# Kernel optimization log

Hardware: AMD Instinct MI355X
Metric: run time of the kernel (lower is better)

The kernel has to match this reference:

```python
import jax, jax.numpy as jnp
import numpy as np

N = 50000      # num nodes
E = 800000     # num edges (before self loops)
HID = 64       # hidden_channels
HEADS = 4
B = 256        # num graphs in batch
TEXT, VIS, AUD = 768, 512, 128


def setup_inputs() -> dict:
    key = jax.random.key(0)
    ks = jax.random.split(key, 24)
    rn = lambda k, shape: jax.random.normal(k, shape, dtype=jnp.float32) * 0.05
    inp = {}
    inp["x"] = jax.random.normal(ks[0], (N, TEXT), dtype=jnp.float32)
    inp["node_type"] = jax.random.randint(ks[1], (N,), 0, 3, dtype=jnp.int32)
    inp["edge_index"] = jax.random.randint(ks[2], (2, E), 0, N, dtype=jnp.int32)
    inp["batch"] = jnp.sort(jax.random.randint(ks[3], (N,), 0, B, dtype=jnp.int32))
    # modality projections
    inp["Wt"] = rn(ks[4], (TEXT, HID)); inp["bt"] = jnp.zeros((HID,), jnp.float32)
    inp["Wv"] = rn(ks[5], (VIS, HID));  inp["bv"] = jnp.zeros((HID,), jnp.float32)
    inp["Wa"] = rn(ks[6], (AUD, HID));  inp["ba"] = jnp.zeros((HID,), jnp.float32)
    # GATConv1: in=HID, out=HID, heads=HEADS, concat=True
    inp["W1"]  = rn(ks[7], (HID, HEADS * HID))
    inp["a1s"] = rn(ks[8], (HEADS, HID))
    inp["a1d"] = rn(ks[9], (HEADS, HID))
    inp["b1"]  = jnp.zeros((HEADS * HID,), jnp.float32)
    # GATConv2: in=HID*HEADS, out=HID, heads=1, concat=False
    inp["W2"]  = rn(ks[10], (HID * HEADS, HID))
    inp["a2s"] = rn(ks[11], (1, HID))
    inp["a2d"] = rn(ks[12], (1, HID))
    inp["b2"]  = jnp.zeros((HID,), jnp.float32)
    # final classifier (num_classes==2 -> out_dim 1, squeezed)
    inp["Wl"] = rn(ks[13], (HID, 1)); inp["bl"] = jnp.zeros((1,), jnp.float32)
    return inp


def gat_conv(x, edge_index, W, a_src, a_dst, bias, concat):
    """PyG-style GATConv (eval mode, add_self_loops=True, shared lin for src/dst)."""
    n = x.shape[0]
    heads, c = a_src.shape
    loops = jnp.arange(n, dtype=edge_index.dtype)
    src = jnp.concatenate([edge_index[0], loops])
    dst = jnp.concatenate([edge_index[1], loops])
    h = (x @ W).reshape(n, heads, c)                       # [N, H, C]
    alpha_s = jnp.einsum('nhc,hc->nh', h, a_src)           # [N, H]
    alpha_d = jnp.einsum('nhc,hc->nh', h, a_dst)
    e = jax.nn.leaky_relu(alpha_s[src] + alpha_d[dst], 0.2)  # [E', H]
    # numerically-stable softmax over incoming edges of each dst node
    m = jax.ops.segment_max(e, dst, num_segments=n)
    e = jnp.exp(e - m[dst])
    denom = jax.ops.segment_sum(e, dst, num_segments=n)
    alpha = e / (denom[dst] + 1e-16)                        # [E', H]
    out = jax.ops.segment_sum(h[src] * alpha[:, :, None], dst, num_segments=n)
    out = out.reshape(n, heads * c) if concat else out.mean(axis=1)
    return out + bias


def reference(x, node_type, edge_index, batch,
              Wt, bt, Wv, bv, Wa, ba,
              W1, a1s, a1d, b1, W2, a2s, a2d, b2, Wl, bl):
    # masked multimodal projection (type 0=text, 1=vision, 2=audio)
    t = x[:, :TEXT] @ Wt + bt
    v = x[:, :VIS] @ Wv + bv
    a = x[:, :AUD] @ Wa + ba
    nt = node_type[:, None]
    h = jnp.where(nt == 0, t, jnp.where(nt == 1, v, a))     # [N, HID]
    h = jax.nn.elu(gat_conv(h, edge_index, W1, a1s, a1d, b1, concat=True))
    h = gat_conv(h, edge_index, W2, a2s, a2d, b2, concat=False)  # [N, HID]
    # global mean pool over graphs
    sums = jax.ops.segment_sum(h, batch, num_segments=B)
    cnts = jax.ops.segment_sum(jnp.ones((h.shape[0], 1), h.dtype), batch, num_segments=B)
    g = sums / jnp.maximum(cnts, 1.0)                       # [B, HID]
    out = (g @ Wl + bl).squeeze(-1)                          # [B] (binary logit)
    return out
```

## Files before the change

kernel.cpp:

```cpp
#include <hip/hip_runtime.h>
#include <cstdint>
#include <cstddef>

#define TEXTD 768
#define VISD  512
#define AUDD  128

__device__ __forceinline__ float wred_sum(float v){
  #pragma unroll
  for (int m = 32; m >= 1; m >>= 1) v += __shfl_xor(v, m, 64);
  return v;
}
__device__ __forceinline__ float wred_max(float v){
  #pragma unroll
  for (int m = 32; m >= 1; m >>= 1) v = fmaxf(v, __shfl_xor(v, m, 64));
  return v;
}

__global__ __launch_bounds__(256) void k_bcount(const int* __restrict__ ntype, int nN, int nblk,
                                                int* __restrict__ bcnt, int* __restrict__ deg){
  int b = blockIdx.x;
  int i = b*256 + threadIdx.x;
  int lane = threadIdx.x & 63, w = threadIdx.x >> 6;
  int ty = (i < nN) ? ntype[i] : -1;
  if (i < nN) deg[i] = 1;
  __shared__ int wc[4][3];
  #pragma unroll
  for (int t = 0; t < 3; t++){
    unsigned long long m = __ballot(ty == t);
    if (lane == 0) wc[w][t] = __popcll(m);
  }
  __syncthreads();
  if (threadIdx.x < 3){
    int t = threadIdx.x;
    bcnt[t*nblk + b] = wc[0][t] + wc[1][t] + wc[2][t] + wc[3][t];
  }
}
__global__ __launch_bounds__(1024) void k_bscan(const int* __restrict__ bcnt, int nblk, int nN,
                                                int* __restrict__ boff, int* __restrict__ toff,
                                                int* __restrict__ tcnt){
  __shared__ int s[2048];
  int n3 = nblk*3;
  int t = threadIdx.x;
  for (int i = t; i < n3; i += 1024) s[i] = bcnt[i];
  __syncthreads();
  if (t == 0){
    int run = 0;
    for (int i = 0; i < n3; i++){ int v = s[i]; s[i] = run; run += v; }
  }
  __syncthreads();
  for (int i = t; i < n3; i += 1024) boff[i] = s[i];
  if (t == 0){
    toff[0] = 0;         toff[1] = s[nblk];           toff[2] = s[2*nblk];
    tcnt[0] = s[nblk];   tcnt[1] = s[2*nblk]-s[nblk]; tcnt[2] = nN - s[2*nblk];
  }
}
__global__ __launch_bounds__(256) void k_bscatter(const int* __restrict__ ntype, int nN, int nblk,
                                                  const int* __restrict__ boff, int* __restrict__ order){
  int b = blockIdx.x;
  int i = b*256 + threadIdx.x;
  int lane = threadIdx.x & 63, w = threadIdx.x >> 6;
  int ty = (i < nN) ? ntype[i] : -1;
  __shared__ int wc[4][3];
  __shared__ int woff[4][3];
  unsigned long long masks[3];
  #pragma unroll
  for (int t = 0; t < 3; t++){
    masks[t] = __ballot(ty == t);
    if (lane == 0) wc[w][t] = __popcll(masks[t]);
  }
  __syncthreads();
  if (threadIdx.x < 3){
    int t = threadIdx.x, run = 0;
    #pragma unroll
    for (int ww = 0; ww < 4; ww++){ woff[ww][t] = run; run += wc[ww][t]; }
  }
  __syncthreads();
  if (ty >= 0){
    int r = __popcll(masks[ty] & ((1ULL << lane) - 1ULL));
    int pos = boff[ty*nblk + b] + woff[w][ty] + r;
    order[pos] = i;
  }
}

__global__ void k_deg_edges(const int* __restrict__ ei, int E, int* __restrict__ deg){
  int i = blockIdx.x*blockDim.x + threadIdx.x;
  if (i < E) atomicAdd(&deg[ei[E + i]], 1);
}
__global__ __launch_bounds__(1024) void k_scan(int* __restrict__ deg, int* __restrict__ off, int n){
  __shared__ int wsum[16];
  __shared__ int carry_s;
  int t = threadIdx.x, lane = t & 63, w = t >> 6;
  if (t == 0) carry_s = 0;
  __syncthreads();
  for (int base = 0; base < n; base += 1024){
    int i = base + t;
    int v = (i < n) ? deg[i] : 0;
    int orig = v;
    #pragma unroll
    for (int o = 1; o < 64; o <<= 1){ int u = __shfl_up(v, o, 64); if (lane >= o) v += u; }
    if (lane == 63) wsum[w] = v;
    __syncthreads();
    if (t < 16){
      int xv = wsum[t];
      #pragma unroll
      for (int o = 1; o < 16; o <<= 1){ int u = __shfl_up(xv, o, 16); if (t >= o) xv += u; }
      wsum[t] = xv;
    }
    __syncthreads();
    int wbase = (w == 0) ? 0 : wsum[w-1];
    int incl = v + wbase;
    int carry = carry_s;
    if (i < n){ int e = carry + incl - orig; off[i] = e; deg[i] = e; }
    __syncthreads();
    if (t == 0) carry_s = carry + wsum[15];
    __syncthreads();
  }
  if (threadIdx.x == 0) off[n] = carry_s;
}
__global__ void k_scatter(const int* __restrict__ ei, int E, int nN,
                          int* __restrict__ pos, int* __restrict__ csr_src){
  int i = blockIdx.x*blockDim.x + threadIdx.x;
  int total = E + nN;
  if (i >= total) return;
  int s, d;
  if (i < E){ s = ei[i]; d = ei[E + i]; } else { s = i - E; d = s; }
  int p = atomicAdd(&pos[d], 1);
  csr_src[p] = s;
}

__global__ __launch_bounds__(256) void k_afold(const float* __restrict__ W1,
    const float* __restrict__ a1s, const float* __restrict__ a1d,
    float* __restrict__ wfs, float* __restrict__ wfd){
  int t = threadIdx.x;
  int k = t & 63, h = t >> 6;
  const float* wr = W1 + (size_t)k*256 + h*64;
  const float* as = a1s + h*64;
  const float* ad = a1d + h*64;
  float s = 0.f, d = 0.f;
  for (int c = 0; c < 64; c += 4){
    float4 w  = *reinterpret_cast<const float4*>(wr + c);
    float4 sa = *reinterpret_cast<const float4*>(as + c);
    float4 da = *reinterpret_cast<const float4*>(ad + c);
    s += w.x*sa.x + w.y*sa.y + w.z*sa.z + w.w*sa.w;
    d += w.x*da.x + w.y*da.y + w.z*da.z + w.w*da.w;
  }
  wfs[k*4 + h] = s;
  wfd[k*4 + h] = d;
}

__global__ __launch_bounds__(256) void k_projgemm(const float* __restrict__ x,
    const int* __restrict__ order, const int* __restrict__ toff, const int* __restrict__ tcnt,
    const float* __restrict__ Wt, const float* __restrict__ bt,
    const float* __restrict__ Wv, const float* __restrict__ bv,
    const float* __restrict__ Wa, const float* __restrict__ ba,
    const float* __restrict__ wfs, const float* __restrict__ wfd,
    float* __restrict__ h0, float* __restrict__ as1, float* __restrict__ ad1){
  int ty = blockIdx.y;
  int cnt = tcnt[ty];
  int tile = blockIdx.x;
  if (tile*64 >= cnt) return;
  const float* W; const float* bias; int dim;
  if (ty == 0)      { W = Wt; bias = bt; dim = TEXTD; }
  else if (ty == 1) { W = Wv; bias = bv; dim = VISD; }
  else              { W = Wa; bias = ba; dim = AUDD; }
  int off = toff[ty];

  __shared__ float xsT[64][68];
  __shared__ float ws [64][68];
  __shared__ int   nid[64];

  int t = threadIdx.x;
  if (t < 64){
    int idx = tile*64 + t;
    nid[t] = (idx < cnt) ? order[off + idx] : -1;
  }
  __syncthreads();

  int node_l = t & 63;
  int ndl = nid[node_l];
  const float* xrow = x + (size_t)(ndl < 0 ? 0 : ndl) * TEXTD;
  int wrow = t >> 2, wu = t & 3;
  int wvq  = t >> 6;
  int n0 = (t & 15)*4, c0 = (t >> 4)*4, qg = t >> 4;
  float acc[4][4] = {};

  for (int k0 = 0; k0 < dim; k0 += 64){
    __syncthreads();
    #pragma unroll
    for (int j = 0; j < 4; j++){
      int f4 = wvq*4 + j;
      float4 v = *reinterpret_cast<const float4*>(xrow + k0 + f4*4);
      xsT[f4*4+0][node_l] = v.x;
      xsT[f4*4+1][node_l] = v.y;
      xsT[f4*4+2][node_l] = v.z;
      xsT[f4*4+3][node_l] = v.w;
    }
    #pragma unroll
    for (int j = 0; j < 4; j++){
      int f4 = j*4 + wu;
      float4 v = *reinterpret_cast<const float4*>(W + (size_t)(k0 + wrow)*64 + f4*4);
      *reinterpret_cast<float4*>(&ws[wrow][f4*4]) = v;
    }
    __syncthreads();
    #pragma unroll 8
    for (int kk = 0; kk < 64; kk++){
      float4 xv = *reinterpret_cast<const float4*>(&xsT[kk][n0]);
      float4 wv = *reinterpret_cast<const float4*>(&ws[kk][c0]);
      float xa[4] = {xv.x, xv.y, xv.z, xv.w};
      float wb[4] = {wv.x, wv.y, wv.z, wv.w};
      #pragma unroll
      for (int i = 0; i < 4; i++)
        #pragma unroll
        for (int j = 0; j < 4; j++)
          acc[i][j] += xa[i] * wb[j];
    }
  }

  float4 b4 = *reinterpret_cast<const float4*>(bias + c0);
  float bb[4] = {b4.x, b4.y, b4.z, b4.w};
  #pragma unroll
  for (int i = 0; i < 4; i++){
    int nd = nid[n0 + i];
    if (nd >= 0){
      float4 o4 = make_float4(acc[i][0]+bb[0], acc[i][1]+bb[1], acc[i][2]+bb[2], acc[i][3]+bb[3]);
      *reinterpret_cast<float4*>(h0 + (size_t)nd*64 + c0) = o4;
    }
  }

  __syncthreads();
  float* spart = &ws [0][0];
  float* dpart = &xsT[0][0];
  float4 wsv[4], wdv[4];
  #pragma unroll
  for (int j = 0; j < 4; j++){
    wsv[j] = *reinterpret_cast<const float4*>(wfs + (c0+j)*4);
    wdv[j] = *reinterpret_cast<const float4*>(wfd + (c0+j)*4);
  }
  #pragma unroll
  for (int i = 0; i < 4; i++){
    float hv[4];
    #pragma unroll
    for (int j = 0; j < 4; j++) hv[j] = acc[i][j] + bb[j];
    float s0v = hv[0]*wsv[0].x + hv[1]*wsv[1].x + hv[2]*wsv[2].x + hv[3]*wsv[3].x;
    float s1v = hv[0]*wsv[0].y + hv[1]*wsv[1].y + hv[2]*wsv[2].y + hv[3]*wsv[3].y;
    float s2v = hv[0]*wsv[0].z + hv[1]*wsv[1].z + hv[2]*wsv[2].z + hv[3]*wsv[3].z;
    float s3v = hv[0]*wsv[0].w + hv[1]*wsv[1].w + hv[2]*wsv[2].w + hv[3]*wsv[3].w;
    float d0v = hv[0]*wdv[0].x + hv[1]*wdv[1].x + hv[2]*wdv[2].x + hv[3]*wdv[3].x;
    float d1v = hv[0]*wdv[0].y + hv[1]*wdv[1].y + hv[2]*wdv[2].y + hv[3]*wdv[3].y;
    float d2v = hv[0]*wdv[0].z + hv[1]*wdv[1].z + hv[2]*wdv[2].z + hv[3]*wdv[3].z;
    float d3v = hv[0]*wdv[0].w + hv[1]*wdv[1].w + hv[2]*wdv[2].w + hv[3]*wdv[3].w;
    int nidx = (n0 + i)*64 + qg*4;
    spart[nidx+0]=s0v; spart[nidx+1]=s1v; spart[nidx+2]=s2v; spart[nidx+3]=s3v;
    dpart[nidx+0]=d0v; dpart[nidx+1]=d1v; dpart[nidx+2]=d2v; dpart[nidx+3]=d3v;
  }
  __syncthreads();
  if (t < 64){
    int nd = nid[t];
    if (nd >= 0){
      float s[4] = {0,0,0,0}, d[4] = {0,0,0,0};
      #pragma unroll
      for (int g = 0; g < 16; g++){
        #pragma unroll
        for (int h = 0; h < 4; h++){
          s[h] += spart[t*64 + g*4 + h];
          d[h] += dpart[t*64 + g*4 + h];
        }
      }
      *reinterpret_cast<float4*>(as1 + (size_t)nd*4) = make_float4(s[0],s[1],s[2],s[3]);
      *reinterpret_cast<float4*>(ad1 + (size_t)nd*4) = make_float4(d[0],d[1],d[2],d[3]);
    }
  }
}

__global__ __launch_bounds__(256) void k_gat1z(const int* __restrict__ off, const int* __restrict__ srcs,
    const float* __restrict__ as1, const float* __restrict__ ad1,
    const float* __restrict__ h0, float* __restrict__ z, int nN){
  int w = threadIdx.x >> 6, L = threadIdx.x & 63;
  int n = blockIdx.x*4 + w;
  __shared__ int   s_src[4][64];
  __shared__ float s_p[4][64][4];
  if (n >= nN) return;
  int hL = L >> 4, c4 = (L & 15)*4;
  float ad[4];
  { float4 a = *reinterpret_cast<const float4*>(ad1 + (size_t)n*4);
    ad[0]=a.x; ad[1]=a.y; ad[2]=a.z; ad[3]=a.w; }
  int s0 = off[n], s1 = off[n+1];
  float m[4] = {-1e30f,-1e30f,-1e30f,-1e30f};
  float den[4] = {0.f,0.f,0.f,0.f};
  float4 acc = make_float4(0.f,0.f,0.f,0.f);
  for (int base = s0; base < s1; base += 64){
    int e = base + L;
    int cl = min(64, s1 - base);
    bool valid = (e < s1);
    int sv = 0; float v[4];
    if (valid){
      sv = srcs[e];
      float4 a = *reinterpret_cast<const float4*>(as1 + (size_t)sv*4);
      float av[4] = {a.x,a.y,a.z,a.w};
      #pragma unroll
      for (int h = 0; h < 4; h++){ float tt = av[h] + ad[h]; v[h] = (tt>0.f)?tt:0.2f*tt; }
    } else {
      #pragma unroll
      for (int h = 0; h < 4; h++) v[h] = -1e30f;
    }
    float sc[4], pv[4];
    #pragma unroll
    for (int h = 0; h < 4; h++){
      float cm = wred_max(v[h]);
      float mn = fmaxf(m[h], cm);
      sc[h] = __expf(m[h] - mn);
      m[h] = mn;
      float p = valid ? __expf(v[h] - mn) : 0.f;
      den[h] = den[h]*sc[h] + wred_sum(p);
      pv[h] = p;
    }
    { float s4 = sc[hL]; acc.x*=s4; acc.y*=s4; acc.z*=s4; acc.w*=s4; }
    if (valid){
      s_src[w][L] = sv;
      *reinterpret_cast<float4*>(&s_p[w][L][0]) = make_float4(pv[0],pv[1],pv[2],pv[3]);
    }
    #pragma unroll 4
    for (int e2 = 0; e2 < cl; e2++){
      int sr = s_src[w][e2];
      float pp = s_p[w][e2][hL];
      float4 hv = *reinterpret_cast<const float4*>(h0 + (size_t)sr*64 + c4);
      acc.x += pp*hv.x; acc.y += pp*hv.y; acc.z += pp*hv.z; acc.w += pp*hv.w;
    }
  }
  float dl = den[hL] + 1e-16f;
  *reinterpret_cast<float4*>(z + (size_t)n*256 + hL*64 + c4) =
      make_float4(acc.x/dl, acc.y/dl, acc.z/dl, acc.w/dl);
}

__global__ __launch_bounds__(256) void k_glin1(const float* __restrict__ z,
    const float* __restrict__ W1, const float* __restrict__ b1,
    float* __restrict__ g1, int nN){
  int tile = blockIdx.x, q = blockIdx.y;
  int base = tile*64;
  __shared__ float xsT[64][68];
  __shared__ float ws [64][68];
  int t = threadIdx.x;
  int row = t >> 2, fq = t & 3;
  {
    int nd = base + row; if (nd >= nN) nd = nN - 1;
    const float* zr = z + (size_t)nd*256 + q*64;
    #pragma unroll
    for (int j = 0; j < 4; j++){
      int f4 = j*4 + fq;
      float4 v = *reinterpret_cast<const float4*>(zr + f4*4);
      xsT[f4*4+0][row] = v.x; xsT[f4*4+1][row] = v.y;
      xsT[f4*4+2][row] = v.z; xsT[f4*4+3][row] = v.w;
    }
  }
  #pragma unroll
  for (int j = 0; j < 4; j++){
    int f4 = j*4 + fq;
    float4 v = *reinterpret_cast<const float4*>(W1 + (size_t)row*256 + q*64 + f4*4);
    *reinterpret_cast<float4*>(&ws[row][f4*4]) = v;
  }
  __syncthreads();

  int n0 = (t & 15)*4, c0 = (t >> 4)*4;
  float acc[4][4] = {};
  #pragma unroll 8
  for (int k = 0; k < 64; k++){
    float4 xv = *reinterpret_cast<const float4*>(&xsT[k][n0]);
    float4 wv = *reinterpret_cast<const float4*>(&ws[k][c0]);
    float xa[4] = {xv.x, xv.y, xv.z, xv.w};
    float wb[4] = {wv.x, wv.y, wv.z, wv.w};
    #pragma unroll
    for (int i = 0; i < 4; i++)
      #pragma unroll
      for (int j = 0; j < 4; j++)
        acc[i][j] += xa[i] * wb[j];
  }
  float4 b4 = *reinterpret_cast<const float4*>(b1 + q*64 + c0);
  float bb[4] = {b4.x, b4.y, b4.z, b4.w};
  #pragma unroll
  for (int i = 0; i < 4; i++){
    int nd = base + n0 + i;
    if (nd < nN){
      float o[4];
      #pragma unroll
      for (int j = 0; j < 4; j++){
        float u = acc[i][j] + bb[j];
        o[j] = (u > 0.f) ? u : expm1f(u);
      }
      *reinterpret_cast<float4*>(g1 + (size_t)nd*256 + q*64 + c0) =
          make_float4(o[0], o[1], o[2], o[3]);
    }
  }
}

__global__ __launch_bounds__(256) void k_lin2t(const float* __restrict__ g1,
    const float* __restrict__ W2, const float* __restrict__ a2s, const float* __restrict__ a2d,
    float* __restrict__ h2, float* __restrict__ as2, float* __restrict__ ad2, int nN){
  int tile = blockIdx.x;
  int base = tile*64;
  __shared__ float xsT[64][68];
  __shared__ float ws [64][68];
  __shared__ float sPart[16][64];
  __shared__ float dPart[16][64];

  int t = threadIdx.x;
  int row = t >> 2, fq = t & 3;
  int ndl = base + row; if (ndl >= nN) ndl = nN - 1;
  const float* gr = g1 + (size_t)ndl*256;
  int n0 = (t & 15)*4, c0 = (t >> 4)*4, qg = t >> 4;
  float acc[4][4] = {};

  for (int k0 = 0; k0 < 256; k0 += 64){
    __syncthreads();
    #pragma unroll
    for (int j = 0; j < 4; j++){
      int f4 = j*4 + fq;
      float4 v = *reinterpret_cast<const float4*>(gr + k0 + f4*4);
      xsT[f4*4+0][row] = v.x; xsT[f4*4+1][row] = v.y;
      xsT[f4*4+2][row] = v.z; xsT[f4*4+3][row] = v.w;
    }
    #pragma unroll
    for (int j = 0; j < 4; j++){
      int f4 = j*4 + fq;
      float4 v = *reinterpret_cast<const float4*>(W2 + (size_t)(k0 + row)*64 + f4*4);
      *reinterpret_cast<float4*>(&ws[row][f4*4]) = v;
    }
    __syncthreads();
    #pragma unroll 8
    for (int k = 0; k < 64; k++){
      float4 xv = *reinterpret_cast<const float4*>(&xsT[k][n0]);
      float4 wv = *reinterpret_cast<const float4*>(&ws[k][c0]);
      float xa[4] = {xv.x, xv.y, xv.z, xv.w};
      float wb[4] = {wv.x, wv.y, wv.z, wv.w};
      #pragma unroll
      for (int i = 0; i < 4; i++)
        #pragma unroll
        for (int j = 0; j < 4; j++)
          acc[i][j] += xa[i] * wb[j];
    }
  }

  float avs[4], avd[4];
  {
    float4 s4 = *reinterpret_cast<const float4*>(a2s + c0);
    float4 d4 = *reinterpret_cast<const float4*>(a2d + c0);
    avs[0]=s4.x; avs[1]=s4.y; avs[2]=s4.z; avs[3]=s4.w;
    avd[0]=d4.x; avd[1]=d4.y; avd[2]=d4.z; avd[3]=d4.w;
  }
  #pragma unroll
  for (int i = 0; i < 4; i++){
    int nd = base + n0 + i;
    float sp = acc[i][0]*avs[0] + acc[i][1]*avs[1] + acc[i][2]*avs[2] + acc[i][3]*avs[3];
    float dp = acc[i][0]*avd[0] + acc[i][1]*avd[1] + acc[i][2]*avd[2] + acc[i][3]*avd[3];
    sPart[qg][n0+i] = sp;
    dPart[qg][n0+i] = dp;
    if (nd < nN){
      float4 o4 = make_float4(acc[i][0], acc[i][1], acc[i][2], acc[i][3]);
      *reinterpret_cast<float4*>(h2 + (size_t)nd*64 + c0) = o4;
    }
  }
  __syncthreads();
  if (t < 64){
    int nd = base + t;
    if (nd < nN){
      float s = 0.f, d = 0.f;
      #pragma unroll
      for (int g = 0; g < 16; g++){ s += sPart[g][t]; d += dPart[g][t]; }
      as2[nd] = s;
      ad2[nd] = d;
    }
  }
}

__global__ __launch_bounds__(256) void k_gat2v(const int* __restrict__ off, const int* __restrict__ srcs,
    const float* __restrict__ as2, const float* __restrict__ ad2,
    const float* __restrict__ h2, const float* __restrict__ b2,
    float* __restrict__ g2, int nN){
  int w = threadIdx.x >> 6, L = threadIdx.x & 63;
  int n = blockIdx.x*4 + w;
  if (n >= nN) return;
  int g = L >> 4, c4 = (L & 15)*4;
  float ad = ad2[n];
  int s0 = off[n], s1 = off[n+1];
  float m = -1e30f, den = 0.f;
  float4 acc = make_float4(0.f,0.f,0.f,0.f);
  for (int base = s0; base < s1; base += 64){
    int e = base + L;
    int cl = min(64, s1 - base);
    bool valid = (e < s1);
    int sv = 0; float v = -1e30f;
    if (valid){
      sv = srcs[e];
      float tt = as2[sv] + ad;
      v = (tt>0.f)?tt:0.2f*tt;
    }
    float cm = wred_max(v);
    float mn = fmaxf(m, cm);
    float sc = __expf(m - mn);
    m = mn;
    float p = valid ? __expf(v - mn) : 0.f;
    den = den*sc + wred_sum(p);
    acc.x*=sc; acc.y*=sc; acc.z*=sc; acc.w*=sc;
    int iters = (cl + 3) >> 2;
    for (int it = 0; it < iters; ++it){
      int e2   = it*4 + g;
      int esrc = (e2 < cl) ? e2 : (cl - 1);
      int   sr = __shfl(sv, esrc, 64);
      float pp = __shfl(p,  esrc, 64);
      if (e2 < cl){
        float4 hv = *reinterpret_cast<const float4*>(h2 + (size_t)sr*64 + c4);
        acc.x += pp*hv.x; acc.y += pp*hv.y; acc.z += pp*hv.z; acc.w += pp*hv.w;
      }
    }
  }
  #pragma unroll
  for (int s = 16; s <= 32; s <<= 1){
    acc.x += __shfl_xor(acc.x, s, 64);
    acc.y += __shfl_xor(acc.y, s, 64);
    acc.z += __shfl_xor(acc.z, s, 64);
    acc.w += __shfl_xor(acc.w, s, 64);
  }
  float dl = den + 1e-16f;
  if (L < 16){
    float4 b4 = *reinterpret_cast<const float4*>(b2 + c4);
    float4 o4 = make_float4(acc.x/dl + b4.x, acc.y/dl + b4.y,
                            acc.z/dl + b4.z, acc.w/dl + b4.w);
    *reinterpret_cast<float4*>(g2 + (size_t)n*64 + c4) = o4;
  }
}

__global__ void k_bstart(const int* __restrict__ batch, int nN, int B, int* __restrict__ bstart){
  int i = blockIdx.x*blockDim.x + threadIdx.x;
  if (i < nN){
    int prev = (i == 0) ? -1 : batch[i-1];
    int cur  = batch[i];
    for (int b = prev+1; b <= cur; b++) bstart[b] = i;
  } else if (i == nN){
    int last = batch[nN-1];
    for (int b = last+1; b <= B; b++) bstart[b] = nN;
  }
}

__global__ __launch_bounds__(64) void k_pool(const float* __restrict__ g2, const int* __restrict__ bstart,
    const float* __restrict__ Wl, const float* __restrict__ bl, float* __restrict__ out, int B){
  int b = blockIdx.x, c = threadIdx.x;
  int r0 = bstart[b], r1 = bstart[b+1];
  float s = 0.f;
  int i = r0;
  for (; i + 4 <= r1; i += 4){
    s += g2[(size_t)(i+0)*64 + c];
    s += g2[(size_t)(i+1)*64 + c];
    s += g2[(size_t)(i+2)*64 + c];
    s += g2[(size_t)(i+3)*64 + c];
  }
  for (; i < r1; i++) s += g2[(size_t)i*64 + c];
  float g = s / fmaxf((float)(r1 - r0), 1.f);
  float v = wred_sum(g * Wl[c]);
  if (c == 0) out[b] = v + bl[0];
}

extern "C" void kernel_launch(void* const* d_in, const int* in_sizes, int n_in,
                              void* d_out, int out_size, void* d_ws, size_t ws_size,
                              hipStream_t stream){
  const float* x    = (const float*)d_in[0];
  const int*   ntyp = (const int*)  d_in[1];
  const int*   ei   = (const int*)  d_in[2];
  const int*   batch= (const int*)  d_in[3];
  const float* Wt = (const float*)d_in[4];
  const float* bt = (const float*)d_in[5];
  const float* Wv = (const float*)d_in[6];
  const float* bv = (const float*)d_in[7];
  const float* Wa = (const float*)d_in[8];
  const float* ba = (const float*)d_in[9];
  const float* W1 = (const float*)d_in[10];
  const float* a1s= (const float*)d_in[11];
  const float* a1d= (const float*)d_in[12];
  const float* b1 = (const float*)d_in[13];
  const float* W2 = (const float*)d_in[14];
  const float* a2s= (const float*)d_in[15];
  const float* a2d= (const float*)d_in[16];
  const float* b2 = (const float*)d_in[17];
  const float* Wl = (const float*)d_in[18];
  const float* bl = (const float*)d_in[19];

  const int N = in_sizes[1];
  const int E = in_sizes[2] / 2;
  const int B = out_size;
  const int nblk = (N + 255)/256;

  char* ws = (char*)d_ws;
  size_t o = 0;
  auto alloc = [&](size_t bytes) -> void* {
    void* p = ws + o;
    o = (o + bytes + 255) & ~(size_t)255;
    return p;
  };
  int*   csr_off = (int*)  alloc((size_t)(N+1)*4);
  int*   pos     = (int*)  alloc((size_t)N*4);
  int*   csr_src = (int*)  alloc((size_t)(E+N)*4);
  float* as1     = (float*)alloc((size_t)N*4*4);
  float* ad1     = (float*)alloc((size_t)N*4*4);
  float* h0      = (float*)alloc((size_t)N*64*4);
  float* zbuf    = (float*)alloc((size_t)N*256*4);
  float* g1      = (float*)alloc((size_t)N*256*4);
  int*   bstart  = (int*)  alloc((size_t)(B+1)*4);
  int*   bcnt    = (int*)  alloc((size_t)nblk*3*4);
  int*   boff    = (int*)  alloc((size_t)nblk*3*4);
  int*   toff    = (int*)  alloc(3*4);
  int*   tcnt    = (int*)  alloc(3*4);
  int*   order   = (int*)  alloc((size_t)N*4);
  float* wfs     = (float*)alloc(256*4);
  float* wfd     = (float*)alloc(256*4);
  float* h2  = h0;
  float* as2 = as1;
  float* ad2 = ad1;
  float* g2  = zbuf;

  k_bcount  <<<nblk, 256, 0, stream>>>(ntyp, N, nblk, bcnt, pos);
  k_bscan   <<<1, 1024, 0, stream>>>(bcnt, nblk, N, boff, toff, tcnt);
  k_bscatter<<<nblk, 256, 0, stream>>>(ntyp, N, nblk, boff, order);

  k_deg_edges<<<(E + 255)/256, 256, 0, stream>>>(ei, E, pos);
  k_scan     <<<1, 1024, 0, stream>>>(pos, csr_off, N);
  k_scatter  <<<(E + N + 255)/256, 256, 0, stream>>>(ei, E, N, pos, csr_src);

  k_bstart<<<(N + 1 + 255)/256, 256, 0, stream>>>(batch, N, B, bstart);

  k_afold<<<1, 256, 0, stream>>>(W1, a1s, a1d, wfs, wfd);

  {
    dim3 g((N + 63)/64, 3);
    k_projgemm<<<g, 256, 0, stream>>>(x, order, toff, tcnt, Wt, bt, Wv, bv, Wa, ba,
                                      wfs, wfd, h0, as1, ad1);
  }

  k_gat1z <<<(N + 3)/4, 256, 0, stream>>>(csr_off, csr_src, as1, ad1, h0, zbuf, N);
  {
    dim3 g((N + 63)/64, 4);
    k_glin1<<<g, 256, 0, stream>>>(zbuf, W1, b1, g1, N);
  }

  k_lin2t<<<(N + 63)/64, 256, 0, stream>>>(g1, W2, a2s, a2d, h2, as2, ad2, N);
  k_gat2v<<<(N + 3)/4, 256, 0, stream>>>(csr_off, csr_src, as2, ad2, h2, b2, g2, N);
  k_pool<<<B, 64, 0, stream>>>(g2, bstart, Wl, bl, (float*)d_out, B);
}
```

Baseline: 390.7 us.

## Fuse GAT1 linear+ELU into layer-2 GEMM and parallelize degree scan

The GAT1 output projection (z·W1 + b1, ELU) is now computed per 64-column chunk in shared memory and fed straight into the W2 GEMM inside one kernel. This removes the 50000x256 g1 intermediate, which was written and then read back in full. The single-block serial prefix scan over node degrees becomes a three-kernel block-sum, small-scan and offset-write scheme that uses many blocks. The trade-offs are extra syncs and smem traffic per chunk in the fused kernel, fewer launched blocks for the first GEMM, and two extra small launches.

```diff
diff --git a/kernel.cpp b/kernel.cpp
--- a/kernel.cpp
+++ b/kernel.cpp
@@ -7,6 +7,11 @@
 #define AUDD  128
 
 __device__ __forceinline__ float wred_sum(float v){
+  #pragma unroll
+  for (int m = 32; m >= 1; m >>= 1) v += __shfl_xor(v, m, 64);
+  return v;
+}
+__device__ __forceinline__ int wred_sumi(int v){
   #pragma unroll
   for (int m = 32; m >= 1; m >>= 1) v += __shfl_xor(v, m, 64);
   return v;
@@ -87,36 +92,53 @@
   int i = blockIdx.x*blockDim.x + threadIdx.x;
   if (i < E) atomicAdd(&deg[ei[E + i]], 1);
 }
-__global__ __launch_bounds__(1024) void k_scan(int* __restrict__ deg, int* __restrict__ off, int n){
+__global__ __launch_bounds__(1024) void k_sumblk(const int* __restrict__ deg, int n,
+                                                 int* __restrict__ bsum){
+  int b = blockIdx.x;
+  int i = b*1024 + threadIdx.x;
+  int lane = threadIdx.x & 63, w = threadIdx.x >> 6;
   __shared__ int wsum[16];
-  __shared__ int carry_s;
+  int v = (i < n) ? deg[i] : 0;
+  v = wred_sumi(v);
+  if (lane == 0) wsum[w] = v;
+  __syncthreads();
+  if (threadIdx.x == 0){
+    int s = 0;
+    #pragma unroll
+    for (int k = 0; k < 16; k++) s += wsum[k];
+    bsum[b] = s;
+  }
+}
+__global__ void k_sumscan(const int* __restrict__ bsum, int nsb, int* __restrict__ bsoff){
+  if (threadIdx.x == 0){
+    int run = 0;
+    for (int i = 0; i < nsb; i++){ bsoff[i] = run; run += bsum[i]; }
+    bsoff[nsb] = run;
+  }
+}
+__global__ __launch_bounds__(1024) void k_offw(int* __restrict__ deg, const int* __restrict__ bsoff,
+                                               int n, int* __restrict__ off){
+  int b = blockIdx.x;
+  int i = b*1024 + threadIdx.x;
   int t = threadIdx.x, lane = t & 63, w = t >> 6;
-  if (t == 0) carry_s = 0;
-  __syncthreads();
-  for (int base = 0; base < n; base += 1024){
-    int i = base + t;
-    int v = (i < n) ? deg[i] : 0;
-    int orig = v;
-    #pragma unroll
-    for (int o = 1; o < 64; o <<= 1){ int u = __shfl_up(v, o, 64); if (lane >= o) v += u; }
-    if (lane == 63) wsum[w] = v;
-    __syncthreads();
-    if (t < 16){
-      int xv = wsum[t];
-      #pragma unroll
-      for (int o = 1; o < 16; o <<= 1){ int u = __shfl_up(xv, o, 16); if (t >= o) xv += u; }
-      wsum[t] = xv;
-    }
-    __syncthreads();
-    int wbase = (w == 0) ? 0 : wsum[w-1];
-    int incl = v + wbase;
-    int carry = carry_s;
-    if (i < n){ int e = carry + incl - orig; off[i] = e; deg[i] = e; }
-    __syncthreads();
-    if (t == 0) carry_s = carry + wsum[15];
-    __syncthreads();
-  }
-  if (threadIdx.x == 0) off[n] = carry_s;
+  __shared__ int wsum[16];
+  int v = (i < n) ? deg[i] : 0;
+  int orig = v;
+  #pragma unroll
+  for (int o = 1; o < 64; o <<= 1){ int u = __shfl_up(v, o, 64); if (lane >= o) v += u; }
+  if (lane == 63) wsum[w] = v;
+  __syncthreads();
+  if (t < 16){
+    int xv = wsum[t];
+    #pragma unroll
+    for (int o = 1; o < 16; o <<= 1){ int u = __shfl_up(xv, o, 16); if (t >= o) xv += u; }
+    wsum[t] = xv;
+  }
+  __syncthreads();
+  int wbase = (w == 0) ? 0 : wsum[w-1];
+  int e = bsoff[b] + v + wbase - orig;
+  if (i < n){ off[i] = e; deg[i] = e; }
+  if (b == 0 && t == 0) off[n] = bsoff[gridDim.x];
 }
 __global__ void k_scatter(const int* __restrict__ ei, int E, int nN,
                           int* __restrict__ pos, int* __restrict__ csr_src){
@@ -333,71 +355,11 @@
       make_float4(acc.x/dl, acc.y/dl, acc.z/dl, acc.w/dl);
 }
 
-__global__ __launch_bounds__(256) void k_glin1(const float* __restrict__ z,
+__global__ __launch_bounds__(256) void k_fuse12(const float* __restrict__ z,
     const float* __restrict__ W1, const float* __restrict__ b1,
-    float* __restrict__ g1, int nN){
-  int tile = blockIdx.x, q = blockIdx.y;
-  int base = tile*64;
-  __shared__ float xsT[64][68];
-  __shared__ float ws [64][68];
-  int t = threadIdx.x;
-  int row = t >> 2, fq = t & 3;
-  {
-    int nd = base + row; if (nd >= nN) nd = nN - 1;
-    const float* zr = z + (size_t)nd*256 + q*64;
-    #pragma unroll
-    for (int j = 0; j < 4; j++){
-      int f4 = j*4 + fq;
-      float4 v = *reinterpret_cast<const float4*>(zr + f4*4);
-      xsT[f4*4+0][row] = v.x; xsT[f4*4+1][row] = v.y;
-      xsT[f4*4+2][row] = v.z; xsT[f4*4+3][row] = v.w;
-    }
-  }
-  #pragma unroll
-  for (int j = 0; j < 4; j++){
-    int f4 = j*4 + fq;
-    float4 v = *reinterpret_cast<const float4*>(W1 + (size_t)row*256 + q*64 + f4*4);
-    *reinterpret_cast<float4*>(&ws[row][f4*4]) = v;
-  }
-  __syncthreads();
-
-  int n0 = (t & 15)*4, c0 = (t >> 4)*4;
-  float acc[4][4] = {};
-  #pragma unroll 8
-  for (int k = 0; k < 64; k++){
-    float4 xv = *reinterpret_cast<const float4*>(&xsT[k][n0]);
-    float4 wv = *reinterpret_cast<const float4*>(&ws[k][c0]);
-    float xa[4] = {xv.x, xv.y, xv.z, xv.w};
-    float wb[4] = {wv.x, wv.y, wv.z, wv.w};
-    #pragma unroll
-    for (int i = 0; i < 4; i++)
-      #pragma unroll
-      for (int j = 0; j < 4; j++)
-        acc[i][j] += xa[i] * wb[j];
-  }
-  float4 b4 = *reinterpret_cast<const float4*>(b1 + q*64 + c0);
-  float bb[4] = {b4.x, b4.y, b4.z, b4.w};
-  #pragma unroll
-  for (int i = 0; i < 4; i++){
-    int nd = base + n0 + i;
-    if (nd < nN){
-      float o[4];
-      #pragma unroll
-      for (int j = 0; j < 4; j++){
-        float u = acc[i][j] + bb[j];
-        o[j] = (u > 0.f) ? u : expm1f(u);
-      }
-      *reinterpret_cast<float4*>(g1 + (size_t)nd*256 + q*64 + c0) =
-          make_float4(o[0], o[1], o[2], o[3]);
-    }
-  }
-}
-
-__global__ __launch_bounds__(256) void k_lin2t(const float* __restrict__ g1,
     const float* __restrict__ W2, const float* __restrict__ a2s, const float* __restrict__ a2d,
     float* __restrict__ h2, float* __restrict__ as2, float* __restrict__ ad2, int nN){
-  int tile = blockIdx.x;
-  int base = tile*64;
+  int base = blockIdx.x*64;
   __shared__ float xsT[64][68];
   __shared__ float ws [64][68];
   __shared__ float sPart[16][64];
@@ -406,23 +368,62 @@
   int t = threadIdx.x;
   int row = t >> 2, fq = t & 3;
   int ndl = base + row; if (ndl >= nN) ndl = nN - 1;
-  const float* gr = g1 + (size_t)ndl*256;
   int n0 = (t & 15)*4, c0 = (t >> 4)*4, qg = t >> 4;
-  float acc[4][4] = {};
-
-  for (int k0 = 0; k0 < 256; k0 += 64){
+  float h2acc[4][4] = {};
+
+  for (int q = 0; q < 4; q++){
     __syncthreads();
+    {
+      const float* zr = z + (size_t)ndl*256 + q*64;
+      #pragma unroll
+      for (int j = 0; j < 4; j++){
+        int f4 = j*4 + fq;
+        float4 v = *reinterpret_cast<const float4*>(zr + f4*4);
+        xsT[f4*4+0][row] = v.x; xsT[f4*4+1][row] = v.y;
+        xsT[f4*4+2][row] = v.z; xsT[f4*4+3][row] = v.w;
+      }
+    }
     #pragma unroll
     for (int j = 0; j < 4; j++){
       int f4 = j*4 + fq;
-      float4 v = *reinterpret_cast<const float4*>(gr + k0 + f4*4);
-      xsT[f4*4+0][row] = v.x; xsT[f4*4+1][row] = v.y;
-      xsT[f4*4+2][row] = v.z; xsT[f4*4+3][row] = v.w;
-    }
+      float4 v = *reinterpret_cast<const float4*>(W1 + (size_t)row*256 + q*64 + f4*4);
+      *reinterpret_cast<float4*>(&ws[row][f4*4]) = v;
+    }
+    __syncthreads();
+    float racc[4][4] = {};
+    #pragma unroll 8
+    for (int k = 0; k < 64; k++){
+      float4 xv = *reinterpret_cast<const float4*>(&xsT[k][n0]);
+      float4 wv = *reinterpret_cast<const float4*>(&ws[k][c0]);
+      float xa[4] = {xv.x, xv.y, xv.z, xv.w};
+      float wb[4] = {wv.x, wv.y, wv.z, wv.w};
+      #pragma unroll
+      for (int i = 0; i < 4; i++)
+        #pragma unroll
+        for (int j = 0; j < 4; j++)
+          racc[i][j] += xa[i] * wb[j];
+    }
+    {
+      float4 b4 = *reinterpret_cast<const float4*>(b1 + q*64 + c0);
+      float bb[4] = {b4.x, b4.y, b4.z, b4.w};
+      #pragma unroll
+      for (int i = 0; i < 4; i++)
+        #pragma unroll
+        for (int j = 0; j < 4; j++){
+          float u = racc[i][j] + bb[j];
+          racc[i][j] = (u > 0.f) ? u : expm1f(u);
+        }
+    }
+    __syncthreads();
+    #pragma unroll
+    for (int i = 0; i < 4; i++)
+      #pragma unroll
+      for (int j = 0; j < 4; j++)
+        xsT[c0+j][n0+i] = racc[i][j];
     #pragma unroll
     for (int j = 0; j < 4; j++){
       int f4 = j*4 + fq;
-      float4 v = *reinterpret_cast<const float4*>(W2 + (size_t)(k0 + row)*64 + f4*4);
+      float4 v = *reinterpret_cast<const float4*>(W2 + (size_t)(q*64 + row)*64 + f4*4);
       *reinterpret_cast<float4*>(&ws[row][f4*4]) = v;
     }
     __syncthreads();
@@ -436,7 +437,7 @@
       for (int i = 0; i < 4; i++)
         #pragma unroll
         for (int j = 0; j < 4; j++)
-          acc[i][j] += xa[i] * wb[j];
+          h2acc[i][j] += xa[i] * wb[j];
     }
   }
 
@@ -450,12 +451,12 @@
   #pragma unroll
   for (int i = 0; i < 4; i++){
     int nd = base + n0 + i;
-    float sp = acc[i][0]*avs[0] + acc[i][1]*avs[1] + acc[i][2]*avs[2] + acc[i][3]*avs[3];
-    float dp = acc[i][0]*avd[0] + acc[i][1]*avd[1] + acc[i][2]*avd[2] + acc[i][3]*avd[3];
+    float sp = h2acc[i][0]*avs[0] + h2acc[i][1]*avs[1] + h2acc[i][2]*avs[2] + h2acc[i][3]*avs[3];
+    float dp = h2acc[i][0]*avd[0] + h2acc[i][1]*avd[1] + h2acc[i][2]*avd[2] + h2acc[i][3]*avd[3];
     sPart[qg][n0+i] = sp;
     dPart[qg][n0+i] = dp;
     if (nd < nN){
-      float4 o4 = make_float4(acc[i][0], acc[i][1], acc[i][2], acc[i][3]);
+      float4 o4 = make_float4(h2acc[i][0], h2acc[i][1], h2acc[i][2], h2acc[i][3]);
       *reinterpret_cast<float4*>(h2 + (size_t)nd*64 + c0) = o4;
     }
   }
@@ -587,6 +588,7 @@
   const int E = in_sizes[2] / 2;
   const int B = out_size;
   const int nblk = (N + 255)/256;
+  const int nsb  = (N + 1023)/1024;
 
   char* ws = (char*)d_ws;
   size_t o = 0;
@@ -602,7 +604,6 @@
   float* ad1     = (float*)alloc((size_t)N*4*4);
   float* h0      = (float*)alloc((size_t)N*64*4);
   float* zbuf    = (float*)alloc((size_t)N*256*4);
-  float* g1      = (float*)alloc((size_t)N*256*4);
   int*   bstart  = (int*)  alloc((size_t)(B+1)*4);
   int*   bcnt    = (int*)  alloc((size_t)nblk*3*4);
   int*   boff    = (int*)  alloc((size_t)nblk*3*4);
@@ -611,6 +612,8 @@
   int*   order   = (int*)  alloc((size_t)N*4);
   float* wfs     = (float*)alloc(256*4);
   float* wfd     = (float*)alloc(256*4);
+  int*   bsum    = (int*)  alloc((size_t)nsb*4);
+  int*   bsoff   = (int*)  alloc((size_t)(nsb+1)*4);
   float* h2  = h0;
   float* as2 = as1;
   float* ad2 = ad1;
@@ -621,8 +624,10 @@
   k_bscatter<<<nblk, 256, 0, stream>>>(ntyp, N, nblk, boff, order);
 
   k_deg_edges<<<(E + 255)/256, 256, 0, stream>>>(ei, E, pos);
-  k_scan     <<<1, 1024, 0, stream>>>(pos, csr_off, N);
-  k_scatter  <<<(E + N + 255)/256, 256, 0, stream>>>(ei, E, N, pos, csr_src);
+  k_sumblk  <<<nsb, 1024, 0, stream>>>(pos, N, bsum);
+  k_sumscan <<<1, 64, 0, stream>>>(bsum, nsb, bsoff);
+  k_offw    <<<nsb, 1024, 0, stream>>>(pos, bsoff, N, csr_off);
+  k_scatter <<<(E + N + 255)/256, 256, 0, stream>>>(ei, E, N, pos, csr_src);
 
   k_bstart<<<(N + 1 + 255)/256, 256, 0, stream>>>(batch, N, B, bstart);
 
@@ -635,12 +640,8 @@
   }
 
   k_gat1z <<<(N + 3)/4, 256, 0, stream>>>(csr_off, csr_src, as1, ad1, h0, zbuf, N);
-  {
-    dim3 g((N + 63)/64, 4);
-    k_glin1<<<g, 256, 0, stream>>>(zbuf, W1, b1, g1, N);
-  }
-
-  k_lin2t<<<(N + 63)/64, 256, 0, stream>>>(g1, W2, a2s, a2d, h2, as2, ad2, N);
+  k_fuse12<<<(N + 63)/64, 256, 0, stream>>>(zbuf, W1, b1, W2, a2s, a2d, h2, as2, ad2, N);
+
   k_gat2v<<<(N + 3)/4, 256, 0, stream>>>(csr_off, csr_src, as2, ad2, h2, b2, g2, N);
   k_pool<<<B, 64, 0, stream>>>(g2, bstart, Wl, bl, (float*)d_out, B);
 }
```

Result: faster. 350.1 us (-10.4%).
